# Kernel optimization log

Hardware: AMD Instinct MI355X
Metric: run time of the kernel (lower is better)

The kernel has to match this reference:

```python
import jax, jax.numpy as jnp
import numpy as np

N_NODES = 50000
N_EDGES = 200000
D_FEAT = 512
D_HID = 1024


def setup_inputs() -> dict:
    key = jax.random.key(0)
    k_x, k_s, k_d, k_w1, k_w2 = jax.random.split(key, 5)
    x = jax.random.normal(k_x, (N_NODES, D_FEAT), dtype=jnp.float32)
    src = jax.random.randint(k_s, (N_EDGES,), 0, N_NODES, dtype=jnp.int64)
    dst = jax.random.randint(k_d, (N_EDGES,), 0, N_NODES, dtype=jnp.int64)
    # MLP params: Linear(2d -> hidden), ReLU, Linear(hidden -> 1)
    W1 = jax.random.normal(k_w1, (2 * D_FEAT, D_HID), dtype=jnp.float32) * (1.0 / np.sqrt(2 * D_FEAT))
    b1 = jnp.zeros((D_HID,), dtype=jnp.float32)
    W2 = jax.random.normal(k_w2, (D_HID, 1), dtype=jnp.float32) * (1.0 / np.sqrt(D_HID))
    b2 = jnp.zeros((1,), dtype=jnp.float32)
    return {"x": x, "src": src, "dst": dst, "W1": W1, "b1": b1, "W2": W2, "b2": b2}


def reference(x, src, dst, W1, b1, W2, b2):
    # Per-edge gather of src/dst node embeddings, concat along feature dim
    h = jnp.concatenate([x[src], x[dst]], axis=1)          # [E, 2d]
    h = jax.nn.relu(h @ W1 + b1)                            # [E, hidden]
    score = h @ W2 + b2                                     # [E, 1]
    return score
```

## Files before the change

kernel.cpp:

```cpp
#include <hip/hip_runtime.h>
#include <cstdint>
#include <cstddef>

typedef __attribute__((ext_vector_type(8))) short short8;
typedef __attribute__((ext_vector_type(4))) float f32x4;

#define D_FEAT 512
#define D_HID  1024
#define NCOL   2048
#define NCHUNK 32

__device__ __forceinline__ unsigned short f2bf(float f) {
    unsigned u = __builtin_bit_cast(unsigned, f);
    u += 0x7FFFu + ((u >> 16) & 1u);
    return (unsigned short)(u >> 16);
}

#define NCAST 12500

__global__ __launch_bounds__(256) void prep_kernel(const float* __restrict__ x,
                                                   unsigned short* __restrict__ xb,
                                                   const float* __restrict__ W1,
                                                   unsigned short* __restrict__ w1t,
                                                   int n) {
    if ((int)blockIdx.x < NCAST) {
        int i = (blockIdx.x * 256 + threadIdx.x) * 8;
        if (i >= n) return;
        const float4* xp = (const float4*)(x + i);
        float4 a = xp[0], b = xp[1];
        short8 o;
        o[0] = (short)f2bf(a.x); o[1] = (short)f2bf(a.y);
        o[2] = (short)f2bf(a.z); o[3] = (short)f2bf(a.w);
        o[4] = (short)f2bf(b.x); o[5] = (short)f2bf(b.y);
        o[6] = (short)f2bf(b.z); o[7] = (short)f2bf(b.w);
        *(short8*)(xb + i) = o;
    } else {
        __shared__ float tile[32][33];
        const int bid2 = blockIdx.x - NCAST;
        const int half = bid2 >> 9;
        const int kb   = ((bid2 >> 5) & 15) * 32;
        const int nb   = (bid2 & 31) * 32;
        const int tx = threadIdx.x & 31, ty = threadIdx.x >> 5;
        #pragma unroll
        for (int i = 0; i < 32; i += 8)
            tile[ty + i][tx] = W1[(size_t)(half * 512 + kb + ty + i) * 1024 + nb + tx];
        __syncthreads();
        #pragma unroll
        for (int i = 0; i < 32; i += 8)
            w1t[(size_t)(half * 1024 + nb + ty + i) * 512 + kb + tx] = f2bf(tile[tx][ty + i]);
    }
}

#define BM 128
#define BN 128
#define BK 64
#define GM 32

__global__ __launch_bounds__(256, 2) void gemm_uv_kernel(
    const unsigned short* __restrict__ xb,
    const unsigned short* __restrict__ w1t,
    const float* __restrict__ b1,
    unsigned char* __restrict__ qUV,
    float* __restrict__ scales,
    int M, int MB)
{
    __shared__ __align__(16) unsigned short smem[16384];
    unsigned short* sA = smem;
    unsigned short* sB = smem + 8192;

    const int NB = NCOL / BN;
    int bid = blockIdx.x;
    int g    = bid / (GM * NB);
    int rem  = bid - g * (GM * NB);
    int base = g * GM;
    int gm   = MB - base; if (gm > GM) gm = GM;
    int mb   = base + rem % gm;
    int nb   = rem / gm;
    const int m0 = mb * BM;
    const int n0 = nb * BN;

    const int tid  = threadIdx.x;
    const int wave = tid >> 6;
    const int lane = tid & 63;
    const int q    = lane >> 4;
    const int l15  = lane & 15;
    const int wm   = (wave >> 1) * 64;
    const int wn   = (wave & 1) * 64;

    const int ar = lane >> 3;
    const int ac = ((lane & 7) ^ ar) * 8;

    const int swz = l15 & 7;
    const int c0 = (q ^ swz) * 8;
    const int c1 = ((q ^ swz) ^ 4) * 8;

    float b1v[4];
    #pragma unroll
    for (int nt = 0; nt < 4; ++nt) {
        int n = n0 + wn + nt * 16 + l15;
        b1v[nt] = (n < D_HID) ? b1[n] : 0.f;
    }

    f32x4 acc[4][4];
    #pragma unroll
    for (int i = 0; i < 4; ++i)
        #pragma unroll
        for (int j = 0; j < 4; ++j)
            acc[i][j] = (f32x4){b1v[j], b1v[j], b1v[j], b1v[j]};

    #pragma unroll 1
    for (int kt = 0; kt < 8; ++kt) {
        const int k0 = kt * BK;
        __syncthreads();
        #pragma unroll
        for (int i = 0; i < 4; ++i) {
            int slot = wave * 4 + i;
            int row  = slot * 8 + ar;
            int m    = m0 + row; if (m >= M) m = M - 1;
            __builtin_amdgcn_global_load_lds(
                (const __attribute__((address_space(1))) void*)(xb + (size_t)m * D_FEAT + k0 + ac),
                (__attribute__((address_space(3))) void*)(sA + slot * 512),
                16, 0, 0);
        }
        #pragma unroll
        for (int i = 0; i < 4; ++i) {
            int slot = wave * 4 + i;
            int row  = slot * 8 + ar;
            __builtin_amdgcn_global_load_lds(
                (const __attribute__((address_space(1))) void*)(w1t + (size_t)(n0 + row) * D_FEAT + k0 + ac),
                (__attribute__((address_space(3))) void*)(sB + slot * 512),
                16, 0, 0);
        }
        __syncthreads();
        {
            short8 a[4], b[4];
            #pragma unroll
            for (int mt = 0; mt < 4; ++mt)
                a[mt] = *(const short8*)(sA + (wm + mt * 16 + l15) * 64 + c0);
            #pragma unroll
            for (int nt = 0; nt < 4; ++nt)
                b[nt] = *(const short8*)(sB + (wn + nt * 16 + l15) * 64 + c0);
            #pragma unroll
            for (int mt = 0; mt < 4; ++mt)
                #pragma unroll
                for (int nt = 0; nt < 4; ++nt)
                    acc[mt][nt] = __builtin_amdgcn_mfma_f32_16x16x32_bf16(a[mt], b[nt], acc[mt][nt], 0, 0, 0);
            #pragma unroll
            for (int mt = 0; mt < 4; ++mt)
                a[mt] = *(const short8*)(sA + (wm + mt * 16 + l15) * 64 + c1);
            #pragma unroll
            for (int nt = 0; nt < 4; ++nt)
                b[nt] = *(const short8*)(sB + (wn + nt * 16 + l15) * 64 + c1);
            #pragma unroll
            for (int mt = 0; mt < 4; ++mt)
                #pragma unroll
                for (int nt = 0; nt < 4; ++nt)
                    acc[mt][nt] = __builtin_amdgcn_mfma_f32_16x16x32_bf16(a[mt], b[nt], acc[mt][nt], 0, 0, 0);
        }
    }

    float msc[4], minv[4];
    #pragma unroll
    for (int mt = 0; mt < 4; ++mt) {
        float m_ = 1e-30f;
        #pragma unroll
        for (int nt = 0; nt < 4; ++nt)
            #pragma unroll
            for (int r = 0; r < 4; ++r)
                m_ = fmaxf(m_, fabsf(acc[mt][nt][r]));
        #pragma unroll
        for (int off = 1; off < 64; off <<= 1)
            m_ = fmaxf(m_, __shfl_xor(m_, off));
        msc[mt]  = m_ * (1.0f / 127.0f);
        minv[mt] = 127.0f * __builtin_amdgcn_rcpf(m_);
    }

    __syncthreads();
    unsigned char* ep8 = (unsigned char*)smem + wave * 4096;
    const float MAGIC = 12583040.0f;
    #pragma unroll
    for (int mt = 0; mt < 4; ++mt)
        #pragma unroll
        for (int nt = 0; nt < 4; ++nt)
            #pragma unroll
            for (int r = 0; r < 4; ++r) {
                float f = fmaf(acc[mt][nt][r], minv[mt], MAGIC);
                ep8[(mt * 16 + q * 4 + r) * 64 + ((nt ^ q) * 16) + l15] =
                    (unsigned char)__builtin_bit_cast(unsigned, f);
            }
    const int chunk = (n0 + wn) >> 6;
    {
        int srow = m0 + wm + q * 16 + l15;
        if (srow < M) scales[(size_t)srow * NCHUNK + chunk] = msc[q];
    }
    #pragma unroll
    for (int i = 0; i < 4; ++i) {
        int flat = i * 64 + lane;
        int r   = flat >> 2;
        int cI  = flat & 3;
        int m   = m0 + wm + r;
        if (m < M) {
            int4 v = *(const int4*)(ep8 + r * 64 + ((cI ^ ((r >> 2) & 3)) * 16));
            *(int4*)(qUV + (size_t)m * NCOL + n0 + wn + cI * 16) = v;
        }
    }
}

__global__ __launch_bounds__(256) void edge_score_kernel(
    const unsigned char* __restrict__ qUV,
    const float* __restrict__ scales,
    const int* __restrict__ src, const int* __restrict__ dst,
    const float* __restrict__ W2, const float* __restrict__ b2,
    float* __restrict__ out, int E)
{
    const int wave = threadIdx.x >> 6;
    const int lane = threadIdx.x & 63;
    const int gw = blockIdx.x * 4 + wave;
    const int ebase = gw * 4;
    if (ebase >= E) return;

    const float4* wp = (const float4*)(W2 + lane * 16);
    float4 wa = wp[0], wb = wp[1], wcv = wp[2], wd = wp[3];
    float w[16] = {wa.x, wa.y, wa.z, wa.w, wb.x, wb.y, wb.z, wb.w,
                   wcv.x, wcv.y, wcv.z, wcv.w, wd.x, wd.y, wd.z, wd.w};
    const float bias = b2[0];
    const int ch = lane >> 2;

    #pragma unroll
    for (int p = 0; p < 2; ++p) {
        const int e0 = ebase + p * 2;
        if (e0 < E) {
            const int e1 = e0 + 1;
            const bool has1 = (e1 < E);

            const int s0 = src[e0];
            const int d0 = dst[e0];
            const int s1 = has1 ? src[e1] : s0;
            const int d1 = has1 ? dst[e1] : d0;

            uint4 qu0 = *(const uint4*)(qUV + (size_t)s0 * NCOL + lane * 16);
            uint4 qv0 = *(const uint4*)(qUV + (size_t)d0 * NCOL + D_HID + lane * 16);
            uint4 qu1 = *(const uint4*)(qUV + (size_t)s1 * NCOL + lane * 16);
            uint4 qv1 = *(const uint4*)(qUV + (size_t)d1 * NCOL + D_HID + lane * 16);
            float su0 = scales[(size_t)s0 * NCHUNK + ch];
            float sv0 = scales[(size_t)d0 * NCHUNK + 16 + ch];
            float su1 = scales[(size_t)s1 * NCHUNK + ch];
            float sv1 = scales[(size_t)d1 * NCHUNK + 16 + ch];
            float cc0 = -128.0f * (su0 + sv0);
            float cc1 = -128.0f * (su1 + sv1);

            const unsigned* u0w = (const unsigned*)&qu0; const unsigned* v0w = (const unsigned*)&qv0;
            const unsigned* u1w = (const unsigned*)&qu1; const unsigned* v1w = (const unsigned*)&qv1;

            float acc0 = 0.f, acc1 = 0.f;
            #pragma unroll
            for (int dw = 0; dw < 4; ++dw) {
                #pragma unroll
                for (int b = 0; b < 4; ++b) {
                    int k = dw * 4 + b;
                    float ub0 = (float)((u0w[dw] >> (8 * b)) & 0xFFu);
                    float vb0 = (float)((v0w[dw] >> (8 * b)) & 0xFFu);
                    float h0 = fmaf(ub0, su0, fmaf(vb0, sv0, cc0));
                    acc0 = fmaf(fmaxf(h0, 0.f), w[k], acc0);
                    float ub1 = (float)((u1w[dw] >> (8 * b)) & 0xFFu);
                    float vb1 = (float)((v1w[dw] >> (8 * b)) & 0xFFu);
                    float h1 = fmaf(ub1, su1, fmaf(vb1, sv1, cc1));
                    acc1 = fmaf(fmaxf(h1, 0.f), w[k], acc1);
                }
            }
            #pragma unroll
            for (int off = 1; off < 64; off <<= 1) {
                acc0 += __shfl_xor(acc0, off);
                acc1 += __shfl_xor(acc1, off);
            }
            if (lane == 0) out[e0] = acc0 + bias;
            if (lane == 1 && has1) out[e1] = acc1 + bias;
        }
    }
}

extern "C" void kernel_launch(void* const* d_in, const int* in_sizes, int n_in,
                              void* d_out, int out_size, void* d_ws, size_t ws_size,
                              hipStream_t stream) {
    const float* x   = (const float*)d_in[0];
    const int*   src = (const int*)d_in[1];
    const int*   dst = (const int*)d_in[2];
    const float* W1  = (const float*)d_in[3];
    const float* b1  = (const float*)d_in[4];
    const float* W2  = (const float*)d_in[5];
    const float* b2  = (const float*)d_in[6];
    float* out = (float*)d_out;

    const int M = in_sizes[0] / D_FEAT;
    const int E = in_sizes[1];

    char* ws = (char*)d_ws;
    unsigned char*  qUV    = (unsigned char*)ws;
    float*          scales = (float*)(ws + (size_t)M * NCOL);
    unsigned short* xb     = (unsigned short*)(ws + (size_t)M * NCOL + (size_t)M * NCHUNK * 4);
    unsigned short* w1t    = (unsigned short*)(ws + (size_t)M * NCOL + (size_t)M * NCHUNK * 4
                                                  + (size_t)M * D_FEAT * 2);

    const int nx = M * D_FEAT;
    prep_kernel<<<NCAST + 1024, 256, 0, stream>>>(x, xb, W1, w1t, nx);

    const int MB  = (M + BM - 1) / BM;
    const int MB0 = MB / 2;
    const int M0  = MB0 * BM;
    gemm_uv_kernel<<<MB0 * (NCOL / BN), 256, 0, stream>>>(
        xb, w1t, b1, qUV, scales, M0, MB0);
    gemm_uv_kernel<<<(MB - MB0) * (NCOL / BN), 256, 0, stream>>>(
        xb + (size_t)M0 * D_FEAT, w1t, b1,
        qUV + (size_t)M0 * NCOL, scales + (size_t)M0 * NCHUNK,
        M - M0, MB - MB0);

    edge_score_kernel<<<(E + 15) / 16, 256, 0, stream>>>(qUV, scales, src, dst, W2, b2, out, E);
}
```

Before: 343.7 us.

## Fuse prep, GEMM and edge scoring into one persistent kernel with grid barriers

Replaces the four launches (prep, two GEMM halves, edge score) with one persistent kernel. It runs grid-stride loops over each phase and separates them with a software grid barrier built on global atomics. The aim is to remove launch gaps and the tail between kernels. In exchange, persistent blocks with launch_bounds(256,3) may lose occupancy, and the barrier relies on every block being co-resident, so it could deadlock if the grid does not fit. The grid size is cached statically.

```diff
diff --git a/kernel.cpp b/kernel.cpp
--- a/kernel.cpp
+++ b/kernel.cpp
@@ -9,6 +9,11 @@
 #define D_HID  1024
 #define NCOL   2048
 #define NCHUNK 32
+
+#define BM 128
+#define BN 128
+#define BK 64
+#define GM 32
 
 __device__ __forceinline__ unsigned short f2bf(float f) {
     unsigned u = __builtin_bit_cast(unsigned, f);
@@ -16,265 +21,288 @@
     return (unsigned short)(u >> 16);
 }
 
-#define NCAST 12500
-
-__global__ __launch_bounds__(256) void prep_kernel(const float* __restrict__ x,
-                                                   unsigned short* __restrict__ xb,
-                                                   const float* __restrict__ W1,
-                                                   unsigned short* __restrict__ w1t,
-                                                   int n) {
-    if ((int)blockIdx.x < NCAST) {
-        int i = (blockIdx.x * 256 + threadIdx.x) * 8;
-        if (i >= n) return;
-        const float4* xp = (const float4*)(x + i);
-        float4 a = xp[0], b = xp[1];
-        short8 o;
-        o[0] = (short)f2bf(a.x); o[1] = (short)f2bf(a.y);
-        o[2] = (short)f2bf(a.z); o[3] = (short)f2bf(a.w);
-        o[4] = (short)f2bf(b.x); o[5] = (short)f2bf(b.y);
-        o[6] = (short)f2bf(b.z); o[7] = (short)f2bf(b.w);
-        *(short8*)(xb + i) = o;
-    } else {
-        __shared__ float tile[32][33];
-        const int bid2 = blockIdx.x - NCAST;
-        const int half = bid2 >> 9;
-        const int kb   = ((bid2 >> 5) & 15) * 32;
-        const int nb   = (bid2 & 31) * 32;
-        const int tx = threadIdx.x & 31, ty = threadIdx.x >> 5;
-        #pragma unroll
-        for (int i = 0; i < 32; i += 8)
-            tile[ty + i][tx] = W1[(size_t)(half * 512 + kb + ty + i) * 1024 + nb + tx];
-        __syncthreads();
-        #pragma unroll
-        for (int i = 0; i < 32; i += 8)
-            w1t[(size_t)(half * 1024 + nb + ty + i) * 512 + kb + tx] = f2bf(tile[tx][ty + i]);
-    }
+__device__ unsigned g_cnt = 0;
+__device__ unsigned g_gen = 0;
+
+__device__ __forceinline__ void grid_barrier() {
+    __syncthreads();
+    if (threadIdx.x == 0) {
+        __threadfence();
+        unsigned gen = __hip_atomic_load(&g_gen, __ATOMIC_RELAXED, __HIP_MEMORY_SCOPE_AGENT);
+        unsigned v   = __hip_atomic_fetch_add(&g_cnt, 1u, __ATOMIC_ACQ_REL, __HIP_MEMORY_SCOPE_AGENT);
+        if (v == gridDim.x - 1) {
+            __hip_atomic_store(&g_cnt, 0u, __ATOMIC_RELAXED, __HIP_MEMORY_SCOPE_AGENT);
+            __hip_atomic_fetch_add(&g_gen, 1u, __ATOMIC_RELEASE, __HIP_MEMORY_SCOPE_AGENT);
+        } else {
+            while (__hip_atomic_load(&g_gen, __ATOMIC_ACQUIRE, __HIP_MEMORY_SCOPE_AGENT) == gen)
+                __builtin_amdgcn_s_sleep(2);
+        }
+        __threadfence();
+    }
+    __syncthreads();
 }
 
-#define BM 128
-#define BN 128
-#define BK 64
-#define GM 32
-
-__global__ __launch_bounds__(256, 2) void gemm_uv_kernel(
-    const unsigned short* __restrict__ xb,
-    const unsigned short* __restrict__ w1t,
+__global__ __launch_bounds__(256, 3) void fused_kernel(
+    const float* __restrict__ x,
+    unsigned short* __restrict__ xb,
+    const float* __restrict__ W1,
+    unsigned short* __restrict__ w1t,
+    const int* __restrict__ src, const int* __restrict__ dst,
     const float* __restrict__ b1,
+    const float* __restrict__ W2, const float* __restrict__ b2,
     unsigned char* __restrict__ qUV,
     float* __restrict__ scales,
-    int M, int MB)
+    float* __restrict__ out,
+    int M, int E, int MB, int ncast, int nx)
 {
     __shared__ __align__(16) unsigned short smem[16384];
-    unsigned short* sA = smem;
-    unsigned short* sB = smem + 8192;
-
-    const int NB = NCOL / BN;
-    int bid = blockIdx.x;
-    int g    = bid / (GM * NB);
-    int rem  = bid - g * (GM * NB);
-    int base = g * GM;
-    int gm   = MB - base; if (gm > GM) gm = GM;
-    int mb   = base + rem % gm;
-    int nb   = rem / gm;
-    const int m0 = mb * BM;
-    const int n0 = nb * BN;
 
     const int tid  = threadIdx.x;
     const int wave = tid >> 6;
     const int lane = tid & 63;
-    const int q    = lane >> 4;
-    const int l15  = lane & 15;
-    const int wm   = (wave >> 1) * 64;
-    const int wn   = (wave & 1) * 64;
-
-    const int ar = lane >> 3;
-    const int ac = ((lane & 7) ^ ar) * 8;
-
-    const int swz = l15 & 7;
-    const int c0 = (q ^ swz) * 8;
-    const int c1 = ((q ^ swz) ^ 4) * 8;
-
-    float b1v[4];
-    #pragma unroll
-    for (int nt = 0; nt < 4; ++nt) {
-        int n = n0 + wn + nt * 16 + l15;
-        b1v[nt] = (n < D_HID) ? b1[n] : 0.f;
-    }
-
-    f32x4 acc[4][4];
-    #pragma unroll
-    for (int i = 0; i < 4; ++i)
-        #pragma unroll
-        for (int j = 0; j < 4; ++j)
-            acc[i][j] = (f32x4){b1v[j], b1v[j], b1v[j], b1v[j]};
-
-    #pragma unroll 1
-    for (int kt = 0; kt < 8; ++kt) {
-        const int k0 = kt * BK;
-        __syncthreads();
-        #pragma unroll
-        for (int i = 0; i < 4; ++i) {
-            int slot = wave * 4 + i;
-            int row  = slot * 8 + ar;
-            int m    = m0 + row; if (m >= M) m = M - 1;
-            __builtin_amdgcn_global_load_lds(
-                (const __attribute__((address_space(1))) void*)(xb + (size_t)m * D_FEAT + k0 + ac),
-                (__attribute__((address_space(3))) void*)(sA + slot * 512),
-                16, 0, 0);
+
+    {
+        const int nprep = ncast + 1024;
+        #pragma unroll 1
+        for (int vb = blockIdx.x; vb < nprep; vb += gridDim.x) {
+            if (vb < ncast) {
+                int i = (vb * 256 + tid) * 8;
+                if (i < nx) {
+                    const float4* xp = (const float4*)(x + i);
+                    float4 a = xp[0], b = xp[1];
+                    short8 o;
+                    o[0] = (short)f2bf(a.x); o[1] = (short)f2bf(a.y);
+                    o[2] = (short)f2bf(a.z); o[3] = (short)f2bf(a.w);
+                    o[4] = (short)f2bf(b.x); o[5] = (short)f2bf(b.y);
+                    o[6] = (short)f2bf(b.z); o[7] = (short)f2bf(b.w);
+                    *(short8*)(xb + i) = o;
+                }
+            } else {
+                float (*tile)[33] = (float (*)[33])smem;
+                const int bid2 = vb - ncast;
+                const int half = bid2 >> 9;
+                const int kb   = ((bid2 >> 5) & 15) * 32;
+                const int nb   = (bid2 & 31) * 32;
+                const int tx = tid & 31, ty = tid >> 5;
+                #pragma unroll
+                for (int i = 0; i < 32; i += 8)
+                    tile[ty + i][tx] = W1[(size_t)(half * 512 + kb + ty + i) * 1024 + nb + tx];
+                __syncthreads();
+                #pragma unroll
+                for (int i = 0; i < 32; i += 8)
+                    w1t[(size_t)(half * 1024 + nb + ty + i) * 512 + kb + tx] = f2bf(tile[tx][ty + i]);
+                __syncthreads();
+            }
         }
-        #pragma unroll
-        for (int i = 0; i < 4; ++i) {
-            int slot = wave * 4 + i;
-            int row  = slot * 8 + ar;
-            __builtin_amdgcn_global_load_lds(
-                (const __attribute__((address_space(1))) void*)(w1t + (size_t)(n0 + row) * D_FEAT + k0 + ac),
-                (__attribute__((address_space(3))) void*)(sB + slot * 512),
-                16, 0, 0);
+    }
+
+    grid_barrier();
+
+    {
+        unsigned short* sA = smem;
+        unsigned short* sB = smem + 8192;
+        const int NB = NCOL / BN;
+        const int ntile = MB * NB;
+
+        const int q    = lane >> 4;
+        const int l15  = lane & 15;
+        const int wm   = (wave >> 1) * 64;
+        const int wn   = (wave & 1) * 64;
+        const int ar   = lane >> 3;
+        const int ac   = ((lane & 7) ^ ar) * 8;
+        const int swz  = l15 & 7;
+        const int c0   = (q ^ swz) * 8;
+        const int c1   = ((q ^ swz) ^ 4) * 8;
+        const float MAGIC = 12583040.0f;
+
+        #pragma unroll 1
+        for (int idx = blockIdx.x; idx < ntile; idx += gridDim.x) {
+            int g    = idx / (GM * NB);
+            int rem  = idx - g * (GM * NB);
+            int base = g * GM;
+            int gm   = MB - base; if (gm > GM) gm = GM;
+            int mb   = base + rem % gm;
+            int nb   = rem / gm;
+            const int m0 = mb * BM;
+            const int n0 = nb * BN;
+
+            float b1v[4];
+            #pragma unroll
+            for (int nt = 0; nt < 4; ++nt) {
+                int n = n0 + wn + nt * 16 + l15;
+                b1v[nt] = (n < D_HID) ? b1[n] : 0.f;
+            }
+            f32x4 acc[4][4];
+            #pragma unroll
+            for (int i = 0; i < 4; ++i)
+                #pragma unroll
+                for (int j = 0; j < 4; ++j)
+                    acc[i][j] = (f32x4){b1v[j], b1v[j], b1v[j], b1v[j]};
+
+            #pragma unroll 1
+            for (int kt = 0; kt < 8; ++kt) {
+                const int k0 = kt * BK;
+                __syncthreads();
+                #pragma unroll
+                for (int i = 0; i < 4; ++i) {
+                    int slot = wave * 4 + i;
+                    int row  = slot * 8 + ar;
+                    int m    = m0 + row; if (m >= M) m = M - 1;
+                    __builtin_amdgcn_global_load_lds(
+                        (const __attribute__((address_space(1))) void*)(xb + (size_t)m * D_FEAT + k0 + ac),
+                        (__attribute__((address_space(3))) void*)(sA + slot * 512),
+                        16, 0, 0);
+                }
+                #pragma unroll
+                for (int i = 0; i < 4; ++i) {
+                    int slot = wave * 4 + i;
+                    int row  = slot * 8 + ar;
+                    __builtin_amdgcn_global_load_lds(
+                        (const __attribute__((address_space(1))) void*)(w1t + (size_t)(n0 + row) * D_FEAT + k0 + ac),
+                        (__attribute__((address_space(3))) void*)(sB + slot * 512),
+                        16, 0, 0);
+                }
+                __syncthreads();
+                {
+                    short8 a[4], b[4];
+                    #pragma unroll
+                    for (int mt = 0; mt < 4; ++mt)
+                        a[mt] = *(const short8*)(sA + (wm + mt * 16 + l15) * 64 + c0);
+                    #pragma unroll
+                    for (int nt = 0; nt < 4; ++nt)
+                        b[nt] = *(const short8*)(sB + (wn + nt * 16 + l15) * 64 + c0);
+                    #pragma unroll
+                    for (int mt = 0; mt < 4; ++mt)
+                        #pragma unroll
+                        for (int nt = 0; nt < 4; ++nt)
+                            acc[mt][nt] = __builtin_amdgcn_mfma_f32_16x16x32_bf16(a[mt], b[nt], acc[mt][nt], 0, 0, 0);
+                    #pragma unroll
+                    for (int mt = 0; mt < 4; ++mt)
+                        a[mt] = *(const short8*)(sA + (wm + mt * 16 + l15) * 64 + c1);
+                    #pragma unroll
+                    for (int nt = 0; nt < 4; ++nt)
+                        b[nt] = *(const short8*)(sB + (wn + nt * 16 + l15) * 64 + c1);
+                    #pragma unroll
+                    for (int mt = 0; mt < 4; ++mt)
+                        #pragma unroll
+                        for (int nt = 0; nt < 4; ++nt)
+                            acc[mt][nt] = __builtin_amdgcn_mfma_f32_16x16x32_bf16(a[mt], b[nt], acc[mt][nt], 0, 0, 0);
+                }
+            }
+
+            float msc[4], minv[4];
+            #pragma unroll
+            for (int mt = 0; mt < 4; ++mt) {
+                float m_ = 1e-30f;
+                #pragma unroll
+                for (int nt = 0; nt < 4; ++nt)
+                    #pragma unroll
+                    for (int r = 0; r < 4; ++r)
+                        m_ = fmaxf(m_, fabsf(acc[mt][nt][r]));
+                #pragma unroll
+                for (int off = 1; off < 64; off <<= 1)
+                    m_ = fmaxf(m_, __shfl_xor(m_, off));
+                msc[mt]  = m_ * (1.0f / 127.0f);
+                minv[mt] = 127.0f * __builtin_amdgcn_rcpf(m_);
+            }
+
+            __syncthreads();
+            unsigned char* ep8 = (unsigned char*)smem + wave * 4096;
+            #pragma unroll
+            for (int mt = 0; mt < 4; ++mt)
+                #pragma unroll
+                for (int nt = 0; nt < 4; ++nt)
+                    #pragma unroll
+                    for (int r = 0; r < 4; ++r) {
+                        float f = fmaf(acc[mt][nt][r], minv[mt], MAGIC);
+                        ep8[(mt * 16 + q * 4 + r) * 64 + ((nt ^ q) * 16) + l15] =
+                            (unsigned char)__builtin_bit_cast(unsigned, f);
+                    }
+            const int chunk = (n0 + wn) >> 6;
+            {
+                int srow = m0 + wm + q * 16 + l15;
+                if (srow < M) scales[(size_t)srow * NCHUNK + chunk] = msc[q];
+            }
+            #pragma unroll
+            for (int i = 0; i < 4; ++i) {
+                int flat = i * 64 + lane;
+                int r   = flat >> 2;
+                int cI  = flat & 3;
+                int m   = m0 + wm + r;
+                if (m < M) {
+                    int4 v = *(const int4*)(ep8 + r * 64 + ((cI ^ ((r >> 2) & 3)) * 16));
+                    *(int4*)(qUV + (size_t)m * NCOL + n0 + wn + cI * 16) = v;
+                }
+            }
         }
-        __syncthreads();
-        {
-            short8 a[4], b[4];
-            #pragma unroll
-            for (int mt = 0; mt < 4; ++mt)
-                a[mt] = *(const short8*)(sA + (wm + mt * 16 + l15) * 64 + c0);
-            #pragma unroll
-            for (int nt = 0; nt < 4; ++nt)
-                b[nt] = *(const short8*)(sB + (wn + nt * 16 + l15) * 64 + c0);
-            #pragma unroll
-            for (int mt = 0; mt < 4; ++mt)
-                #pragma unroll
-                for (int nt = 0; nt < 4; ++nt)
-                    acc[mt][nt] = __builtin_amdgcn_mfma_f32_16x16x32_bf16(a[mt], b[nt], acc[mt][nt], 0, 0, 0);
-            #pragma unroll
-            for (int mt = 0; mt < 4; ++mt)
-                a[mt] = *(const short8*)(sA + (wm + mt * 16 + l15) * 64 + c1);
-            #pragma unroll
-            for (int nt = 0; nt < 4; ++nt)
-                b[nt] = *(const short8*)(sB + (wn + nt * 16 + l15) * 64 + c1);
-            #pragma unroll
-            for (int mt = 0; mt < 4; ++mt)
-                #pragma unroll
-                for (int nt = 0; nt < 4; ++nt)
-                    acc[mt][nt] = __builtin_amdgcn_mfma_f32_16x16x32_bf16(a[mt], b[nt], acc[mt][nt], 0, 0, 0);
-        }
-    }
-
-    float msc[4], minv[4];
-    #pragma unroll
-    for (int mt = 0; mt < 4; ++mt) {
-        float m_ = 1e-30f;
-        #pragma unroll
-        for (int nt = 0; nt < 4; ++nt)
-            #pragma unroll
-            for (int r = 0; r < 4; ++r)
-                m_ = fmaxf(m_, fabsf(acc[mt][nt][r]));
-        #pragma unroll
-        for (int off = 1; off < 64; off <<= 1)
-            m_ = fmaxf(m_, __shfl_xor(m_, off));
-        msc[mt]  = m_ * (1.0f / 127.0f);
-        minv[mt] = 127.0f * __builtin_amdgcn_rcpf(m_);
-    }
-
-    __syncthreads();
-    unsigned char* ep8 = (unsigned char*)smem + wave * 4096;
-    const float MAGIC = 12583040.0f;
-    #pragma unroll
-    for (int mt = 0; mt < 4; ++mt)
-        #pragma unroll
-        for (int nt = 0; nt < 4; ++nt)
-            #pragma unroll
-            for (int r = 0; r < 4; ++r) {
-                float f = fmaf(acc[mt][nt][r], minv[mt], MAGIC);
-                ep8[(mt * 16 + q * 4 + r) * 64 + ((nt ^ q) * 16) + l15] =
-                    (unsigned char)__builtin_bit_cast(unsigned, f);
-            }
-    const int chunk = (n0 + wn) >> 6;
+    }
+
+    grid_barrier();
+
     {
-        int srow = m0 + wm + q * 16 + l15;
-        if (srow < M) scales[(size_t)srow * NCHUNK + chunk] = msc[q];
-    }
-    #pragma unroll
-    for (int i = 0; i < 4; ++i) {
-        int flat = i * 64 + lane;
-        int r   = flat >> 2;
-        int cI  = flat & 3;
-        int m   = m0 + wm + r;
-        if (m < M) {
-            int4 v = *(const int4*)(ep8 + r * 64 + ((cI ^ ((r >> 2) & 3)) * 16));
-            *(int4*)(qUV + (size_t)m * NCOL + n0 + wn + cI * 16) = v;
-        }
-    }
-}
-
-__global__ __launch_bounds__(256) void edge_score_kernel(
-    const unsigned char* __restrict__ qUV,
-    const float* __restrict__ scales,
-    const int* __restrict__ src, const int* __restrict__ dst,
-    const float* __restrict__ W2, const float* __restrict__ b2,
-    float* __restrict__ out, int E)
-{
-    const int wave = threadIdx.x >> 6;
-    const int lane = threadIdx.x & 63;
-    const int gw = blockIdx.x * 4 + wave;
-    const int ebase = gw * 4;
-    if (ebase >= E) return;
-
-    const float4* wp = (const float4*)(W2 + lane * 16);
-    float4 wa = wp[0], wb = wp[1], wcv = wp[2], wd = wp[3];
-    float w[16] = {wa.x, wa.y, wa.z, wa.w, wb.x, wb.y, wb.z, wb.w,
-                   wcv.x, wcv.y, wcv.z, wcv.w, wd.x, wd.y, wd.z, wd.w};
-    const float bias = b2[0];
-    const int ch = lane >> 2;
-
-    #pragma unroll
-    for (int p = 0; p < 2; ++p) {
-        const int e0 = ebase + p * 2;
-        if (e0 < E) {
-            const int e1 = e0 + 1;
-            const bool has1 = (e1 < E);
-
-            const int s0 = src[e0];
-            const int d0 = dst[e0];
-            const int s1 = has1 ? src[e1] : s0;
-            const int d1 = has1 ? dst[e1] : d0;
-
-            uint4 qu0 = *(const uint4*)(qUV + (size_t)s0 * NCOL + lane * 16);
-            uint4 qv0 = *(const uint4*)(qUV + (size_t)d0 * NCOL + D_HID + lane * 16);
-            uint4 qu1 = *(const uint4*)(qUV + (size_t)s1 * NCOL + lane * 16);
-            uint4 qv1 = *(const uint4*)(qUV + (size_t)d1 * NCOL + D_HID + lane * 16);
-            float su0 = scales[(size_t)s0 * NCHUNK + ch];
-            float sv0 = scales[(size_t)d0 * NCHUNK + 16 + ch];
-            float su1 = scales[(size_t)s1 * NCHUNK + ch];
-            float sv1 = scales[(size_t)d1 * NCHUNK + 16 + ch];
-            float cc0 = -128.0f * (su0 + sv0);
-            float cc1 = -128.0f * (su1 + sv1);
-
-            const unsigned* u0w = (const unsigned*)&qu0; const unsigned* v0w = (const unsigned*)&qv0;
-            const unsigned* u1w = (const unsigned*)&qu1; const unsigned* v1w = (const unsigned*)&qv1;
-
-            float acc0 = 0.f, acc1 = 0.f;
-            #pragma unroll
-            for (int dw = 0; dw < 4; ++dw) {
-                #pragma unroll
-                for (int b = 0; b < 4; ++b) {
-                    int k = dw * 4 + b;
-                    float ub0 = (float)((u0w[dw] >> (8 * b)) & 0xFFu);
-                    float vb0 = (float)((v0w[dw] >> (8 * b)) & 0xFFu);
-                    float h0 = fmaf(ub0, su0, fmaf(vb0, sv0, cc0));
-                    acc0 = fmaf(fmaxf(h0, 0.f), w[k], acc0);
-                    float ub1 = (float)((u1w[dw] >> (8 * b)) & 0xFFu);
-                    float vb1 = (float)((v1w[dw] >> (8 * b)) & 0xFFu);
-                    float h1 = fmaf(ub1, su1, fmaf(vb1, sv1, cc1));
-                    acc1 = fmaf(fmaxf(h1, 0.f), w[k], acc1);
-                }
-            }
-            #pragma unroll
-            for (int off = 1; off < 64; off <<= 1) {
-                acc0 += __shfl_xor(acc0, off);
-                acc1 += __shfl_xor(acc1, off);
-            }
-            if (lane == 0) out[e0] = acc0 + bias;
-            if (lane == 1 && has1) out[e1] = acc1 + bias;
+        const int nvb = (E + 15) / 16;
+
+        const float4* wp = (const float4*)(W2 + lane * 16);
+        float4 wa = wp[0], wb = wp[1], wcv = wp[2], wd = wp[3];
+        float w[16] = {wa.x, wa.y, wa.z, wa.w, wb.x, wb.y, wb.z, wb.w,
+                       wcv.x, wcv.y, wcv.z, wcv.w, wd.x, wd.y, wd.z, wd.w};
+        const float bias = b2[0];
+        const int ch = lane >> 2;
+
+        #pragma unroll 1
+        for (int vb = blockIdx.x; vb < nvb; vb += gridDim.x) {
+            const int ebase = (vb * 4 + wave) * 4;
+            #pragma unroll
+            for (int p = 0; p < 2; ++p) {
+                const int e0 = ebase + p * 2;
+                if (e0 < E) {
+                    const int e1 = e0 + 1;
+                    const bool has1 = (e1 < E);
+
+                    const int s0 = src[e0];
+                    const int d0 = dst[e0];
+                    const int s1 = has1 ? src[e1] : s0;
+                    const int d1 = has1 ? dst[e1] : d0;
+
+                    uint4 qu0 = *(const uint4*)(qUV + (size_t)s0 * NCOL + lane * 16);
+                    uint4 qv0 = *(const uint4*)(qUV + (size_t)d0 * NCOL + D_HID + lane * 16);
+                    uint4 qu1 = *(const uint4*)(qUV + (size_t)s1 * NCOL + lane * 16);
+                    uint4 qv1 = *(const uint4*)(qUV + (size_t)d1 * NCOL + D_HID + lane * 16);
+                    float su0 = scales[(size_t)s0 * NCHUNK + ch];
+                    float sv0 = scales[(size_t)d0 * NCHUNK + 16 + ch];
+                    float su1 = scales[(size_t)s1 * NCHUNK + ch];
+                    float sv1 = scales[(size_t)d1 * NCHUNK + 16 + ch];
+                    float cc0 = -128.0f * (su0 + sv0);
+                    float cc1 = -128.0f * (su1 + sv1);
+
+                    const unsigned* u0w = (const unsigned*)&qu0; const unsigned* v0w = (const unsigned*)&qv0;
+                    const unsigned* u1w = (const unsigned*)&qu1; const unsigned* v1w = (const unsigned*)&qv1;
+
+                    float acc0 = 0.f, acc1 = 0.f;
+                    #pragma unroll
+                    for (int dw = 0; dw < 4; ++dw) {
+                        #pragma unroll
+                        for (int b = 0; b < 4; ++b) {
+                            int k = dw * 4 + b;
+                            float ub0 = (float)((u0w[dw] >> (8 * b)) & 0xFFu);
+                            float vb0 = (float)((v0w[dw] >> (8 * b)) & 0xFFu);
+                            float h0 = fmaf(ub0, su0, fmaf(vb0, sv0, cc0));
+                            acc0 = fmaf(fmaxf(h0, 0.f), w[k], acc0);
+                            float ub1 = (float)((u1w[dw] >> (8 * b)) & 0xFFu);
+                            float vb1 = (float)((v1w[dw] >> (8 * b)) & 0xFFu);
+                            float h1 = fmaf(ub1, su1, fmaf(vb1, sv1, cc1));
+                            acc1 = fmaf(fmaxf(h1, 0.f), w[k], acc1);
+                        }
+                    }
+                    #pragma unroll
+                    for (int off = 1; off < 64; off <<= 1) {
+                        acc0 += __shfl_xor(acc0, off);
+                        acc1 += __shfl_xor(acc1, off);
+                    }
+                    if (lane == 0) out[e0] = acc0 + bias;
+                    if (lane == 1 && has1) out[e1] = acc1 + bias;
+                }
+            }
         }
     }
 }
@@ -301,18 +329,27 @@
     unsigned short* w1t    = (unsigned short*)(ws + (size_t)M * NCOL + (size_t)M * NCHUNK * 4
                                                   + (size_t)M * D_FEAT * 2);
 
-    const int nx = M * D_FEAT;
-    prep_kernel<<<NCAST + 1024, 256, 0, stream>>>(x, xb, W1, w1t, nx);
-
-    const int MB  = (M + BM - 1) / BM;
-    const int MB0 = MB / 2;
-    const int M0  = MB0 * BM;
-    gemm_uv_kernel<<<MB0 * (NCOL / BN), 256, 0, stream>>>(
-        xb, w1t, b1, qUV, scales, M0, MB0);
-    gemm_uv_kernel<<<(MB - MB0) * (NCOL / BN), 256, 0, stream>>>(
-        xb + (size_t)M0 * D_FEAT, w1t, b1,
-        qUV + (size_t)M0 * NCOL, scales + (size_t)M0 * NCHUNK,
-        M - M0, MB - MB0);
-
-    edge_score_kernel<<<(E + 15) / 16, 256, 0, stream>>>(qUV, scales, src, dst, W2, b2, out, E);
+    int nx    = M * D_FEAT;
+    int ncast = (nx / 8 + 255) / 256;
+    int MB    = (M + BM - 1) / BM;
+
+    static int g_grid = 0;
+    if (g_grid == 0) {
+        int occ = 0;
+        if (hipOccupancyMaxActiveBlocksPerMultiprocessor(&occ, fused_kernel, 256, 0) != hipSuccess || occ < 1)
+            occ = 1;
+        int dev = 0, ncu = 256;
+        hipGetDevice(&dev);
+        hipDeviceProp_t prop;
+        if (hipGetDeviceProperties(&prop, dev) == hipSuccess && prop.multiProcessorCount > 0)
+            ncu = prop.multiProcessorCount;
+        long g = (long)occ * ncu;
+        if (g > 768) g = 768;
+        if (g < 8)   g = 8;
+        g_grid = (int)g;
+    }
+
+    fused_kernel<<<g_grid, 256, 0, stream>>>(
+        x, xb, W1, w1t, src, dst, b1, W2, b2, qUV, scales, out,
+        M, E, MB, ncast, nx);
 }
```

Result: slower. 624.5 us (+81.7%).
